# Kernel optimization log

Hardware: AMD Instinct MI355X
Metric: run time of the kernel (lower is better)

## Reference

```python
import jax, jax.numpy as jnp
import numpy as np

D = 1024
H = 16
MODES = 16
EPS = 1e-5


def _layernorm(x, g, b):
    mu = jnp.mean(x, axis=-1, keepdims=True)
    var = jnp.var(x, axis=-1, keepdims=True)
    return (x - mu) * jax.lax.rsqrt(var + EPS) * g + b


def setup_inputs() -> dict:
    key = jax.random.key(0)
    ks = jax.random.split(key, 12)
    B, S = 32, 2048
    x_feat = jax.random.normal(ks[0], (B, S, D), dtype=jnp.float32)
    z_prev = jax.random.normal(ks[1], (B, D), dtype=jnp.float32)
    # MultiheadAttention params (torch packs q,k,v in in_proj)
    in_proj_w = jax.random.normal(ks[2], (3 * D, D), dtype=jnp.float32) * (1.0 / np.sqrt(D))
    in_proj_b = jnp.zeros((3 * D,), dtype=jnp.float32)
    out_proj_w = jax.random.normal(ks[3], (D, D), dtype=jnp.float32) * (1.0 / np.sqrt(D))
    out_proj_b = jnp.zeros((D,), dtype=jnp.float32)
    ln1_g = jnp.ones((D,), jnp.float32); ln1_b = jnp.zeros((D,), jnp.float32)
    ln2_g = jnp.ones((D,), jnp.float32); ln2_b = jnp.zeros((D,), jnp.float32)
    scale_real = jax.random.normal(ks[4], (MODES, D), dtype=jnp.float32) * 0.02
    scale_imag = jax.random.normal(ks[5], (MODES, D), dtype=jnp.float32) * 0.02
    # spectral_norm(Linear): effective weight = W / sigma_max(W); bake it in
    Wp = np.asarray(jax.random.normal(ks[6], (D, D), dtype=jnp.float32)) * (1.0 / np.sqrt(D))
    sigma = np.linalg.svd(Wp, compute_uv=False)[0]
    proj_w = jnp.asarray(Wp / sigma, dtype=jnp.float32)
    proj_b = jnp.zeros((D,), jnp.float32)
    bn_g = jnp.ones((D,), jnp.float32); bn_b = jnp.zeros((D,), jnp.float32)
    gate = jnp.asarray(0.5, jnp.float32)
    scale_attn = jnp.ones((1,), jnp.float32)
    scale_denoise = jnp.ones((1,), jnp.float32)
    return dict(x_feat=x_feat, z_prev=z_prev, in_proj_w=in_proj_w, in_proj_b=in_proj_b,
                out_proj_w=out_proj_w, out_proj_b=out_proj_b, ln1_g=ln1_g, ln1_b=ln1_b,
                ln2_g=ln2_g, ln2_b=ln2_b, scale_real=scale_real, scale_imag=scale_imag,
                proj_w=proj_w, proj_b=proj_b, bn_g=bn_g, bn_b=bn_b, gate=gate,
                scale_attn=scale_attn, scale_denoise=scale_denoise)


def reference(x_feat, z_prev, in_proj_w, in_proj_b, out_proj_w, out_proj_b,
              ln1_g, ln1_b, ln2_g, ln2_b, scale_real, scale_imag,
              proj_w, proj_b, bn_g, bn_b, gate, scale_attn, scale_denoise):
    B, S, _ = x_feat.shape
    hd = D // H
    Wq, Wk, Wv = in_proj_w[:D], in_proj_w[D:2 * D], in_proj_w[2 * D:]
    bq, bk, bv = in_proj_b[:D], in_proj_b[D:2 * D], in_proj_b[2 * D:]
    # single-query cross attention: q from z_prev [B,D], k/v from x_feat [B,S,D]
    q = (z_prev @ Wq.T + bq).reshape(B, H, hd)
    k = (x_feat @ Wk.T + bk).reshape(B, S, H, hd)
    v = (x_feat @ Wv.T + bv).reshape(B, S, H, hd)
    scores = jnp.einsum('bhd,bshd->bhs', q, k) / np.sqrt(hd)
    attn = jax.nn.softmax(scores, axis=-1)
    ctx = jnp.einsum('bhs,bshd->bhd', attn, v).reshape(B, D)
    attn_out = ctx @ out_proj_w.T + out_proj_b
    z1 = _layernorm(z_prev + scale_attn * attn_out, ln1_g, ln1_b)  # [B,D]
    # fft_denoise: keep first MODES freqs, each scaled by mean of its complex filter row
    filt = jnp.mean(scale_real + 1j * scale_imag, axis=1)  # [MODES] complex
    fvec = jnp.zeros((D,), dtype=jnp.complex64).at[:MODES].set(filt.astype(jnp.complex64))
    z_freq = jnp.fft.fft(z1, axis=1) * fvec[None, :]
    z_spatial = jnp.fft.ifft(z_freq, axis=1).real.astype(z1.dtype)
    denoised = z_spatial @ proj_w.T + proj_b
    z2 = _layernorm(z1 + scale_denoise * denoised, ln2_g, ln2_b)
    g = jax.nn.sigmoid(gate)
    z3 = g * z2 + (1.0 - g) * z_prev
    # BatchNorm1d (training-mode batch stats, biased variance)
    mu = jnp.mean(z3, axis=0, keepdims=True)
    var = jnp.var(z3, axis=0, keepdims=True)
    out = (z3 - mu) * jax.lax.rsqrt(var + EPS) * bn_g + bn_b
    return out
```

## Files before the change

kernel.cpp:

```cpp
#include <hip/hip_runtime.h>
#include <hip/hip_bf16.h>

#define B_ 32
#define S_ 2048
#define D_ 1024
#define H_ 16
#define HD_ 64
#define MODES_ 16
#define EPS_ 1e-5f

#define NSPLIT_ 16
#define RPB_ 128
#define RPI_ 16
#define NIT_ (RPB_ / RPI_)

#define OFF_CK      32
#define OFF_Q       1024
#define OFF_QKBF    33792
#define OFF_ML      295936
#define ML_L_OFF    8192
#define OFF_PART_F  312320
#define OFF_CTX     4506624
#define OFF_R1      4539392
#define OFF_Z1      4572160
#define OFF_ZSP     4604928
#define OFF_R2      4637696
#define OFF_Z3      4670464

typedef __attribute__((ext_vector_type(8))) short short8v;
typedef __attribute__((ext_vector_type(4))) float f32x4;

static __device__ inline ushort2 f2bf2(float a, float b) {
    __hip_bfloat162 h = __float22bfloat162_rn(make_float2(a, b));
    union { __hip_bfloat162 h; ushort2 u; } v; v.h = h; return v.u;
}
static __device__ inline unsigned short f2bf(float a) {
    __hip_bfloat16 h = __float2bfloat16(a);
    union { __hip_bfloat16 h; unsigned short u; } v; v.h = h; return v.u;
}
static __device__ inline float bf2f(unsigned s) {
    union { unsigned u; float f; } v; v.u = s << 16;
    return v.f;
}

__global__ void k_q(const float* __restrict__ zprev, const float* __restrict__ ipw,
                    const float* __restrict__ ipb, float* __restrict__ q_out,
                    float* __restrict__ ck_out) {
    int b = blockIdx.x >> 2, nc = blockIdx.x & 3;
    __shared__ float zr[D_];
    int t = threadIdx.x;
    for (int i = t; i < D_; i += 256) zr[i] = zprev[(size_t)b * D_ + i];
    __syncthreads();
    int n = nc * 256 + t;
    const float4* wr = (const float4*)(ipw + (size_t)n * D_);
    float a0 = 0.f, a1 = 0.f, a2 = 0.f, a3 = 0.f;
    for (int k = 0; k < 256; k += 4) {
        float4 w0 = wr[k], w1 = wr[k + 1], w2 = wr[k + 2], w3 = wr[k + 3];
        float4 z0 = *(const float4*)&zr[4 * k];
        float4 z1 = *(const float4*)&zr[4 * k + 4];
        float4 z2 = *(const float4*)&zr[4 * k + 8];
        float4 z3 = *(const float4*)&zr[4 * k + 12];
        a0 = fmaf(z0.x, w0.x, a0); a0 = fmaf(z0.y, w0.y, a0); a0 = fmaf(z0.z, w0.z, a0); a0 = fmaf(z0.w, w0.w, a0);
        a1 = fmaf(z1.x, w1.x, a1); a1 = fmaf(z1.y, w1.y, a1); a1 = fmaf(z1.z, w1.z, a1); a1 = fmaf(z1.w, w1.w, a1);
        a2 = fmaf(z2.x, w2.x, a2); a2 = fmaf(z2.y, w2.y, a2); a2 = fmaf(z2.z, w2.z, a2); a2 = fmaf(z2.w, w2.w, a2);
        a3 = fmaf(z3.x, w3.x, a3); a3 = fmaf(z3.y, w3.y, a3); a3 = fmaf(z3.z, w3.z, a3); a3 = fmaf(z3.w, w3.w, a3);
    }
    float qv = (a0 + a1) + (a2 + a3) + ipb[n];
    q_out[(size_t)b * D_ + n] = qv;
    float cv = qv * ipb[D_ + n];
#pragma unroll
    for (int o = 32; o > 0; o >>= 1) cv += __shfl_xor(cv, o);
    if ((t & 63) == 0) ck_out[b * H_ + (n >> 6)] = cv;
}

__global__ void k_qkc(const float* __restrict__ ipw, const float* __restrict__ q_in,
                      unsigned short* __restrict__ qk_out) {
    int bid = blockIdx.x;
    int bc = bid & 3, nc = (bid >> 2) & 3, h = bid >> 4;
    int t = threadIdx.x;
    __shared__ float4 tile4[HD_ * 64];
    __shared__ float qall[8 * HD_];
    const float4* wk4 = (const float4*)(ipw + (size_t)D_ * D_);
#pragma unroll
    for (int j = 0; j < 16; ++j) {
        int lin4 = j * 256 + t;
        int i = lin4 >> 6, n4 = lin4 & 63;
        tile4[lin4] = wk4[(size_t)(h * HD_ + i) * 256 + nc * 64 + n4];
    }
#pragma unroll
    for (int j = 0; j < 2; ++j) {
        int idx = j * 256 + t;
        int bb = idx >> 6, i = idx & 63;
        qall[idx] = q_in[(size_t)(bc * 8 + bb) * D_ + h * HD_ + i];
    }
    __syncthreads();
    const float* tile = (const float*)tile4;
#pragma unroll
    for (int bb = 0; bb < 8; ++bb) {
        float a0 = 0.f, a1 = 0.f;
#pragma unroll
        for (int i = 0; i < HD_; i += 2) {
            a0 = fmaf(qall[bb * HD_ + i], tile[i * 256 + t], a0);
            a1 = fmaf(qall[bb * HD_ + i + 1], tile[(i + 1) * 256 + t], a1);
        }
        int b = bc * 8 + bb;
        qk_out[(size_t)(b * H_ + h) * D_ + nc * 256 + t] = f2bf(a0 + a1);
    }
}

__global__ __launch_bounds__(256, 2) void k_attn(const float* __restrict__ xfeat,
        const unsigned short* __restrict__ qkbf, const float* __restrict__ ck,
        unsigned short* __restrict__ part, float* __restrict__ ml) {
    int bid = blockIdx.x;
    int c = bid & (NSPLIT_ - 1), b = bid >> 4;
    int t = threadIdx.x, w = t >> 6, l = t & 63;
    __shared__ unsigned char xbuf[RPI_ * 2048];
    __shared__ unsigned char xcol[D_ * RPI_ * 2];
    __shared__ float Sred[4][RPI_][17];
    __shared__ unsigned short Pt[16][32];
    __shared__ float mh[16], lh[16], fh[16], ckl[16];

    if (t < 16) { mh[t] = -1e30f; lh[t] = 0.f; ckl[t] = ck[b * H_ + t]; }
    {
        int h = t >> 4, s = 16 + (t & 15);
        Pt[h][s] = 0;
    }

    f32x4 acc[16];
#pragma unroll
    for (int nt = 0; nt < 16; ++nt) acc[nt] = (f32x4){0.f, 0.f, 0.f, 0.f};

    int hr = l & 15, kg = l >> 4;
    const unsigned short* qkb = qkbf + ((size_t)(b * H_ + hr) << 10);
    short8v qfrag[8];
#pragma unroll
    for (int ks = 0; ks < 8; ++ks)
        qfrag[ks] = *(const short8v*)(qkb + w * 256 + ks * 32 + kg * 8);

    for (int it = 0; it < NIT_; ++it) {
        __syncthreads();
        {
            const float4* src = (const float4*)(xfeat + ((size_t)b * S_ + c * RPB_ + it * RPI_) * D_);
#pragma unroll
            for (int j = 0; j < 16; ++j) {
                int idx = j * 256 + t;
                float4 v = src[idx];
                int row = idx >> 8, dq = idx & 255;
                unsigned off = (unsigned)(row * 2048 + dq * 8) ^ (unsigned)((row & 7) << 4);
                ushort2 lo = f2bf2(v.x, v.y), hi = f2bf2(v.z, v.w);
                ushort4 u; u.x = lo.x; u.y = lo.y; u.z = hi.x; u.w = hi.y;
                *(ushort4*)(xbuf + off) = u;
            }
        }
        __syncthreads();
        {
            f32x4 s0 = {0.f, 0.f, 0.f, 0.f};
#pragma unroll
            for (int ks = 0; ks < 8; ++ks) {
                int k = w * 256 + ks * 32 + kg * 8;
                unsigned off0 = (unsigned)(hr * 2048 + k * 2) ^ (unsigned)((hr & 7) << 4);
                short8v a0 = *(const short8v*)(xbuf + off0);
                s0 = __builtin_amdgcn_mfma_f32_16x16x32_bf16(a0, qfrag[ks], s0, 0, 0, 0);
            }
            int rbase = kg * 4;
#pragma unroll
            for (int r = 0; r < 4; ++r) Sred[w][rbase + r][hr] = s0[r];
        }
        {
#pragma unroll
            for (int i = 0; i < 16; ++i) {
                int rg = i & 3, d = (i >> 2) * 256 + t;
                unsigned cb = (unsigned)((d >> 2) * 8) + (unsigned)((d & 3) * 2);
                int r0 = rg * 4;
                unsigned short v0 = *(const unsigned short*)(xbuf + (((unsigned)((r0 + 0) * 2048) + cb) ^ (unsigned)(((r0 + 0) & 7) << 4)));
                unsigned short v1 = *(const unsigned short*)(xbuf + (((unsigned)((r0 + 1) * 2048) + cb) ^ (unsigned)(((r0 + 1) & 7) << 4)));
                unsigned short v2 = *(const unsigned short*)(xbuf + (((unsigned)((r0 + 2) * 2048) + cb) ^ (unsigned)(((r0 + 2) & 7) << 4)));
                unsigned short v3 = *(const unsigned short*)(xbuf + (((unsigned)((r0 + 3) * 2048) + cb) ^ (unsigned)(((r0 + 3) & 7) << 4)));
                ushort4 u; u.x = v0; u.y = v1; u.z = v2; u.w = v3;
                unsigned slot = (unsigned)((rg >> 1) ^ ((d >> 2) & 1));
                unsigned coff = (unsigned)(d * 32) + slot * 16 + (unsigned)((rg & 1) * 8);
                *(ushort4*)(xcol + coff) = u;
            }
        }
        __syncthreads();
        {
            int h = t >> 4, i16 = t & 15;
            float sv0 = Sred[0][i16][h] + Sred[1][i16][h] + Sred[2][i16][h] + Sred[3][i16][h];
            float s0 = (sv0 + ckl[h]) * 0.125f;
            float mm = s0;
#pragma unroll
            for (int o = 8; o > 0; o >>= 1) mm = fmaxf(mm, __shfl_xor(mm, o, 16));
            float mold = mh[h];
            float mnew = fmaxf(mold, mm);
            float p0 = __expf(s0 - mnew);
            Pt[h][i16] = f2bf(p0);
            float ps = p0;
#pragma unroll
            for (int o = 8; o > 0; o >>= 1) ps += __shfl_xor(ps, o, 16);
            if (i16 == 0) {
                float f = __expf(mold - mnew);
                fh[h] = f; lh[h] = lh[h] * f + ps; mh[h] = mnew;
            }
        }
        __syncthreads();
        {
            float f0 = fh[kg * 4 + 0], f1 = fh[kg * 4 + 1], f2 = fh[kg * 4 + 2], f3 = fh[kg * 4 + 3];
#pragma unroll
            for (int nt = 0; nt < 16; ++nt) {
                acc[nt][0] *= f0; acc[nt][1] *= f1; acc[nt][2] *= f2; acc[nt][3] *= f3;
            }
            short8v pa = *(const short8v*)(&Pt[hr][kg * 8]);
#pragma unroll
            for (int nt = 0; nt < 16; ++nt) {
                int d = w * 256 + nt * 16 + hr;
                unsigned coff = (unsigned)(d * 32) + (unsigned)((((kg & 1) ^ ((d >> 2) & 1)) << 4));
                short8v bx = *(const short8v*)(xcol + coff);
                acc[nt] = __builtin_amdgcn_mfma_f32_16x16x32_bf16(pa, bx, acc[nt], 0, 0, 0);
            }
        }
    }
    {
#pragma unroll
        for (int nt = 0; nt < 16; ++nt) {
            int d = w * 256 + nt * 16 + hr;
#pragma unroll
            for (int r = 0; r < 4; ++r) {
                int h = kg * 4 + r;
                part[(((size_t)(c * B_ + b) * H_ + h) << 10) + d] = f2bf(acc[nt][r]);
            }
        }
        if (t < 16) {
            ml[(size_t)(c * B_ + b) * H_ + t] = mh[t];
            ml[ML_L_OFF + (size_t)(c * B_ + b) * H_ + t] = lh[t];
        }
    }
}

__global__ void k_ctx2(const float* __restrict__ ipw, const float* __restrict__ ipb,
                       const unsigned short* __restrict__ part, const float* __restrict__ ml,
                       float* __restrict__ ctx) {
    int b = blockIdx.x >> 2, nc = blockIdx.x & 3;
    int t = threadIdx.x;
    __shared__ float mls[4][16], lls[4][16], coef[4][16];
    __shared__ float xr[4 * D_];
    if (t < 64) {
        int h4 = t >> 4, c = t & 15;
        mls[h4][c] = ml[(size_t)(c * B_ + b) * H_ + nc * 4 + h4];
        lls[h4][c] = ml[ML_L_OFF + (size_t)(c * B_ + b) * H_ + nc * 4 + h4];
    }
    __syncthreads();
    if (t < 4) {
        float M = -1e30f;
        for (int c = 0; c < 16; ++c) M = fmaxf(M, mls[t][c]);
        float L = 0.f;
        for (int c = 0; c < 16; ++c) L += lls[t][c] * __expf(mls[t][c] - M);
        float invL = 1.f / L;
        for (int c = 0; c < 16; ++c) coef[t][c] = __expf(mls[t][c] - M) * invL;
    }
    __syncthreads();
    for (int idx = t * 2; idx < 4 * D_; idx += 512) {
        int h4 = idx >> 10, d = idx & 1023;
        int h = nc * 4 + h4;
        float a0 = 0.f, a1 = 0.f;
        for (int c = 0; c < 16; ++c) {
            unsigned u = *(const unsigned*)&part[(((size_t)(c * B_ + b) * H_ + h) << 10) + d];
            float cf = coef[h4][c];
            a0 = fmaf(bf2f(u & 0xffffu), cf, a0);
            a1 = fmaf(bf2f(u >> 16), cf, a1);
        }
        xr[idx] = a0; xr[idx + 1] = a1;
    }
    __syncthreads();
    int n = nc * 256 + t;
    int hl = t >> 6;
    const float4* wr = (const float4*)(ipw + ((size_t)2 * D_ + n) * D_);
    const float4* xv4 = (const float4*)&xr[hl * D_];
    float a0 = 0.f, a1 = 0.f, a2 = 0.f, a3 = 0.f;
    for (int k = 0; k < 256; k += 4) {
        float4 w0 = wr[k], w1 = wr[k + 1], w2 = wr[k + 2], w3 = wr[k + 3];
        float4 x0 = xv4[k], x1 = xv4[k + 1], x2 = xv4[k + 2], x3 = xv4[k + 3];
        a0 = fmaf(w0.x, x0.x, a0); a0 = fmaf(w0.y, x0.y, a0); a0 = fmaf(w0.z, x0.z, a0); a0 = fmaf(w0.w, x0.w, a0);
        a1 = fmaf(w1.x, x1.x, a1); a1 = fmaf(w1.y, x1.y, a1); a1 = fmaf(w1.z, x1.z, a1); a1 = fmaf(w1.w, x1.w, a1);
        a2 = fmaf(w2.x, x2.x, a2); a2 = fmaf(w2.y, x2.y, a2); a2 = fmaf(w2.z, x2.z, a2); a2 = fmaf(w2.w, x2.w, a2);
        a3 = fmaf(w3.x, x3.x, a3); a3 = fmaf(w3.y, x3.y, a3); a3 = fmaf(w3.z, x3.z, a3); a3 = fmaf(w3.w, x3.w, a3);
    }
    ctx[(size_t)b * D_ + n] = (a0 + a1) + (a2 + a3) + ipb[2 * D_ + n];
}

__global__ void k_proj_res(const float* __restrict__ wmat, const float* __restrict__ bias,
                           const float* __restrict__ scale, const float* __restrict__ resid,
                           const float* __restrict__ invec, float* __restrict__ outvec) {
    int b = blockIdx.x >> 2, nc = blockIdx.x & 3;
    __shared__ float cx[D_];
    int t = threadIdx.x;
    for (int i = t; i < D_; i += 256) cx[i] = invec[(size_t)b * D_ + i];
    __syncthreads();
    int n = nc * 256 + t;
    const float4* wr = (const float4*)(wmat + (size_t)n * D_);
    float a0 = 0.f, a1 = 0.f, a2 = 0.f, a3 = 0.f;
    for (int k = 0; k < 256; k += 4) {
        float4 w0 = wr[k], w1 = wr[k + 1], w2 = wr[k + 2], w3 = wr[k + 3];
        float4 c0 = *(const float4*)&cx[4 * k];
        float4 c1 = *(const float4*)&cx[4 * k + 4];
        float4 c2 = *(const float4*)&cx[4 * k + 8];
        float4 c3 = *(const float4*)&cx[4 * k + 12];
        a0 = fmaf(w0.x, c0.x, a0); a0 = fmaf(w0.y, c0.y, a0); a0 = fmaf(w0.z, c0.z, a0); a0 = fmaf(w0.w, c0.w, a0);
        a1 = fmaf(w1.x, c1.x, a1); a1 = fmaf(w1.y, c1.y, a1); a1 = fmaf(w1.z, c1.z, a1); a1 = fmaf(w1.w, c1.w, a1);
        a2 = fmaf(w2.x, c2.x, a2); a2 = fmaf(w2.y, c2.y, a2); a2 = fmaf(w2.z, c2.z, a2); a2 = fmaf(w2.w, c2.w, a2);
        a3 = fmaf(w3.x, c3.x, a3); a3 = fmaf(w3.y, c3.y, a3); a3 = fmaf(w3.z, c3.z, a3); a3 = fmaf(w3.w, c3.w, a3);
    }
    float acc = (a0 + a1) + (a2 + a3);
    outvec[(size_t)b * D_ + n] = resid[(size_t)b * D_ + n] + scale[0] * (acc + bias[n]);
}

__global__ void k_lnspec(const float* __restrict__ r1, const float* __restrict__ g1,
                         const float* __restrict__ b1, const float* __restrict__ sreal,
                         const float* __restrict__ simag, float* __restrict__ z1out,
                         float* __restrict__ zspout) {
    int b = blockIdx.x, t = threadIdx.x, w = t >> 6, l = t & 63;
    __shared__ float zr[D_];
    __shared__ float fre[MODES_], fim[MODES_];
    __shared__ float cre[MODES_], cim[MODES_];
    __shared__ float sa[4], sb[4];
    float4 v = ((const float4*)(r1 + (size_t)b * D_))[t];
    float s = v.x + v.y + v.z + v.w;
    float s2 = v.x * v.x + v.y * v.y + v.z * v.z + v.w * v.w;
#pragma unroll
    for (int o = 32; o > 0; o >>= 1) { s += __shfl_xor(s, o); s2 += __shfl_xor(s2, o); }
    if (l == 0) { sa[w] = s; sb[w] = s2; }
    int m = t >> 4, sub = t & 15;
    {
        float ar = 0.f, ai = 0.f;
        for (int k = sub; k < D_; k += 16) { ar += sreal[m * D_ + k]; ai += simag[m * D_ + k]; }
#pragma unroll
        for (int o = 8; o > 0; o >>= 1) { ar += __shfl_xor(ar, o, 16); ai += __shfl_xor(ai, o, 16); }
        if (sub == 0) { fre[m] = ar * (1.f / (float)D_); fim[m] = ai * (1.f / (float)D_); }
    }
    __syncthreads();
    s = sa[0] + sa[1] + sa[2] + sa[3];
    s2 = sb[0] + sb[1] + sb[2] + sb[3];
    float mu = s * (1.f / (float)D_);
    float var = s2 * (1.f / (float)D_) - mu * mu;
    float rs = rsqrtf(var + EPS_);
    float4 gg = ((const float4*)g1)[t], bbv = ((const float4*)b1)[t];
    float4 z4;
    z4.x = (v.x - mu) * rs * gg.x + bbv.x;
    z4.y = (v.y - mu) * rs * gg.y + bbv.y;
    z4.z = (v.z - mu) * rs * gg.z + bbv.z;
    z4.w = (v.w - mu) * rs * gg.w + bbv.w;
    ((float4*)(z1out + (size_t)b * D_))[t] = z4;
    *(float4*)&zr[4 * t] = z4;
    __syncthreads();
    const float step = 6.283185307179586f / (float)D_;
    {
        float ar = 0.f, ai = 0.f;
        for (int n = sub; n < D_; n += 16) {
            int idx = (m * n) & (D_ - 1);
            float sn, cs;
            __sincosf(step * (float)idx, &sn, &cs);
            float z = zr[n];
            ar = fmaf(z, cs, ar); ai = fmaf(-z, sn, ai);
        }
#pragma unroll
        for (int o = 8; o > 0; o >>= 1) { ar += __shfl_xor(ar, o, 16); ai += __shfl_xor(ai, o, 16); }
        if (sub == 0) {
            cre[m] = (fre[m] * ar - fim[m] * ai) * (1.f / (float)D_);
            cim[m] = (fre[m] * ai + fim[m] * ar) * (1.f / (float)D_);
        }
    }
    __syncthreads();
    for (int n = t; n < D_; n += 256) {
        float acc = 0.f;
#pragma unroll
        for (int mm = 0; mm < MODES_; ++mm) {
            int idx = (mm * n) & (D_ - 1);
            float sn, cs;
            __sincosf(step * (float)idx, &sn, &cs);
            acc += cre[mm] * cs - cim[mm] * sn;
        }
        zspout[(size_t)b * D_ + n] = acc;
    }
}

__global__ void k_ln2gate(const float* __restrict__ zprev, const float* __restrict__ g2,
                          const float* __restrict__ b2v, const float* __restrict__ gate,
                          float* __restrict__ ws) {
    int b = blockIdx.x, t = threadIdx.x, w = t >> 6, l = t & 63;
    float4 v = ((const float4*)(ws + OFF_R2 + (size_t)b * D_))[t];
    float s = v.x + v.y + v.z + v.w;
    float s2 = v.x * v.x + v.y * v.y + v.z * v.z + v.w * v.w;
    __shared__ float sa[4], sb[4];
#pragma unroll
    for (int o = 32; o > 0; o >>= 1) { s += __shfl_xor(s, o); s2 += __shfl_xor(s2, o); }
    if (l == 0) { sa[w] = s; sb[w] = s2; }
    __syncthreads();
    s = sa[0] + sa[1] + sa[2] + sa[3];
    s2 = sb[0] + sb[1] + sb[2] + sb[3];
    float mu = s * (1.f / (float)D_);
    float var = s2 * (1.f / (float)D_) - mu * mu;
    float rs = rsqrtf(var + EPS_);
    float4 gg = ((const float4*)g2)[t], bb = ((const float4*)b2v)[t];
    float gsig = 1.f / (1.f + __expf(-gate[0]));
    float4 zp = ((const float4*)(zprev + (size_t)b * D_))[t];
    float4 z3;
    z3.x = gsig * ((v.x - mu) * rs * gg.x + bb.x) + (1.f - gsig) * zp.x;
    z3.y = gsig * ((v.y - mu) * rs * gg.y + bb.y) + (1.f - gsig) * zp.y;
    z3.z = gsig * ((v.z - mu) * rs * gg.z + bb.z) + (1.f - gsig) * zp.z;
    z3.w = gsig * ((v.w - mu) * rs * gg.w + bb.w) + (1.f - gsig) * zp.w;
    ((float4*)(ws + OFF_Z3 + (size_t)b * D_))[t] = z3;
}

__global__ void k_bn(const float* __restrict__ bng, const float* __restrict__ bnb,
                     const float* __restrict__ z3, float* __restrict__ out) {
    int d = blockIdx.x * 256 + threadIdx.x;
    float vals[B_];
    float s = 0.f, s2 = 0.f;
#pragma unroll
    for (int b = 0; b < B_; ++b) {
        float v = z3[(size_t)b * D_ + d];
        vals[b] = v; s += v; s2 = fmaf(v, v, s2);
    }
    float mu = s * (1.f / (float)B_);
    float var = s2 * (1.f / (float)B_) - mu * mu;
    float rs = rsqrtf(var + EPS_);
    float gg = bng[d], bb = bnb[d];
#pragma unroll
    for (int b = 0; b < B_; ++b) out[(size_t)b * D_ + d] = (vals[b] - mu) * rs * gg + bb;
}

extern "C" void kernel_launch(void* const* d_in, const int* in_sizes, int n_in,
                              void* d_out, int out_size, void* d_ws, size_t ws_size,
                              hipStream_t stream) {
    const float* x_feat = (const float*)d_in[0];
    const float* z_prev = (const float*)d_in[1];
    const float* ipw    = (const float*)d_in[2];
    const float* ipb    = (const float*)d_in[3];
    const float* wout   = (const float*)d_in[4];
    const float* bout   = (const float*)d_in[5];
    const float* ln1g   = (const float*)d_in[6];
    const float* ln1b   = (const float*)d_in[7];
    const float* ln2g   = (const float*)d_in[8];
    const float* ln2b   = (const float*)d_in[9];
    const float* sreal  = (const float*)d_in[10];
    const float* simag  = (const float*)d_in[11];
    const float* pw     = (const float*)d_in[12];
    const float* pb     = (const float*)d_in[13];
    const float* bng    = (const float*)d_in[14];
    const float* bnb    = (const float*)d_in[15];
    const float* gate   = (const float*)d_in[16];
    const float* sattn  = (const float*)d_in[17];
    const float* sden   = (const float*)d_in[18];
    float* ws  = (float*)d_ws;
    float* out = (float*)d_out;
    unsigned short* qkbf  = (unsigned short*)(ws + OFF_QKBF);
    unsigned short* partp = (unsigned short*)(ws + OFF_PART_F);

    k_q<<<B_ * 4, 256, 0, stream>>>(z_prev, ipw, ipb, ws + OFF_Q, ws + OFF_CK);
    k_qkc<<<H_ * 16, 256, 0, stream>>>(ipw, ws + OFF_Q, qkbf);
    k_attn<<<B_ * NSPLIT_, 256, 0, stream>>>(x_feat, qkbf, ws + OFF_CK, partp, ws + OFF_ML);
    k_ctx2<<<B_ * 4, 256, 0, stream>>>(ipw, ipb, partp, ws + OFF_ML, ws + OFF_CTX);
    k_proj_res<<<B_ * 4, 256, 0, stream>>>(wout, bout, sattn, z_prev, ws + OFF_CTX, ws + OFF_R1);
    k_lnspec<<<B_, 256, 0, stream>>>(ws + OFF_R1, ln1g, ln1b, sreal, simag,
                                     ws + OFF_Z1, ws + OFF_ZSP);
    k_proj_res<<<B_ * 4, 256, 0, stream>>>(pw, pb, sden, ws + OFF_Z1, ws + OFF_ZSP, ws + OFF_R2);
    k_ln2gate<<<B_, 256, 0, stream>>>(z_prev, ln2g, ln2b, gate, ws);
    k_bn<<<D_ / 256, 256, 0, stream>>>(bng, bnb, ws + OFF_Z3, out);
}
```

Measured before the change: 224.1 us.

## Widen attention and GEMV kernels to 512 threads, prefetch next x tile into registers

The split-K attention kernel now runs 8 waves per block, each covering half the previous K/D slice. It loads the next 16-row x_feat tile into registers while the current tile is converted and consumed, so global loads overlap compute. The ctx and projection GEMV kernels also move to 512 threads, splitting each dot product across two lanes joined with a shuffle. The aim is more memory parallelism and latency hiding, at the cost of extra register pressure from the prefetch buffer, an 8-way Sred reduction, and a launch bound of 4 blocks per SM that may be hard to meet with shared memory use.

```diff
diff --git a/kernel.cpp b/kernel.cpp
--- a/kernel.cpp
+++ b/kernel.cpp
@@ -108,7 +108,7 @@
     }
 }
 
-__global__ __launch_bounds__(256, 2) void k_attn(const float* __restrict__ xfeat,
+__global__ __launch_bounds__(512, 4) void k_attn(const float* __restrict__ xfeat,
         const unsigned short* __restrict__ qkbf, const float* __restrict__ ck,
         unsigned short* __restrict__ part, float* __restrict__ ml) {
     int bid = blockIdx.x;
@@ -116,48 +116,54 @@
     int t = threadIdx.x, w = t >> 6, l = t & 63;
     __shared__ unsigned char xbuf[RPI_ * 2048];
     __shared__ unsigned char xcol[D_ * RPI_ * 2];
-    __shared__ float Sred[4][RPI_][17];
+    __shared__ float Sred[8][RPI_][17];
     __shared__ unsigned short Pt[16][32];
     __shared__ float mh[16], lh[16], fh[16], ckl[16];
 
     if (t < 16) { mh[t] = -1e30f; lh[t] = 0.f; ckl[t] = ck[b * H_ + t]; }
-    {
+    if (t < 256) {
         int h = t >> 4, s = 16 + (t & 15);
         Pt[h][s] = 0;
     }
 
-    f32x4 acc[16];
-#pragma unroll
-    for (int nt = 0; nt < 16; ++nt) acc[nt] = (f32x4){0.f, 0.f, 0.f, 0.f};
+    f32x4 acc[8];
+#pragma unroll
+    for (int nt = 0; nt < 8; ++nt) acc[nt] = (f32x4){0.f, 0.f, 0.f, 0.f};
 
     int hr = l & 15, kg = l >> 4;
     const unsigned short* qkb = qkbf + ((size_t)(b * H_ + hr) << 10);
-    short8v qfrag[8];
-#pragma unroll
-    for (int ks = 0; ks < 8; ++ks)
-        qfrag[ks] = *(const short8v*)(qkb + w * 256 + ks * 32 + kg * 8);
+    short8v qfrag[4];
+#pragma unroll
+    for (int ks = 0; ks < 4; ++ks)
+        qfrag[ks] = *(const short8v*)(qkb + w * 128 + ks * 32 + kg * 8);
+
+    const float4* xbase = (const float4*)(xfeat + ((size_t)b * S_ + c * RPB_) * D_);
+    float4 cur[8];
+#pragma unroll
+    for (int j = 0; j < 8; ++j) cur[j] = xbase[j * 512 + t];
 
     for (int it = 0; it < NIT_; ++it) {
         __syncthreads();
-        {
-            const float4* src = (const float4*)(xfeat + ((size_t)b * S_ + c * RPB_ + it * RPI_) * D_);
-#pragma unroll
-            for (int j = 0; j < 16; ++j) {
-                int idx = j * 256 + t;
-                float4 v = src[idx];
-                int row = idx >> 8, dq = idx & 255;
-                unsigned off = (unsigned)(row * 2048 + dq * 8) ^ (unsigned)((row & 7) << 4);
-                ushort2 lo = f2bf2(v.x, v.y), hi = f2bf2(v.z, v.w);
-                ushort4 u; u.x = lo.x; u.y = lo.y; u.z = hi.x; u.w = hi.y;
-                *(ushort4*)(xbuf + off) = u;
-            }
+#pragma unroll
+        for (int j = 0; j < 8; ++j) {
+            int idx = j * 512 + t;
+            int row = idx >> 8, dq = idx & 255;
+            unsigned off = (unsigned)(row * 2048 + dq * 8) ^ (unsigned)((row & 7) << 4);
+            ushort2 lo = f2bf2(cur[j].x, cur[j].y), hi = f2bf2(cur[j].z, cur[j].w);
+            ushort4 u; u.x = lo.x; u.y = lo.y; u.z = hi.x; u.w = hi.y;
+            *(ushort4*)(xbuf + off) = u;
+        }
+        if (it + 1 < NIT_) {
+            const float4* src = xbase + (size_t)(it + 1) * (RPI_ * D_ / 4);
+#pragma unroll
+            for (int j = 0; j < 8; ++j) cur[j] = src[j * 512 + t];
         }
         __syncthreads();
         {
             f32x4 s0 = {0.f, 0.f, 0.f, 0.f};
 #pragma unroll
-            for (int ks = 0; ks < 8; ++ks) {
-                int k = w * 256 + ks * 32 + kg * 8;
+            for (int ks = 0; ks < 4; ++ks) {
+                int k = w * 128 + ks * 32 + kg * 8;
                 unsigned off0 = (unsigned)(hr * 2048 + k * 2) ^ (unsigned)((hr & 7) << 4);
                 short8v a0 = *(const short8v*)(xbuf + off0);
                 s0 = __builtin_amdgcn_mfma_f32_16x16x32_bf16(a0, qfrag[ks], s0, 0, 0, 0);
@@ -168,8 +174,8 @@
         }
         {
 #pragma unroll
-            for (int i = 0; i < 16; ++i) {
-                int rg = i & 3, d = (i >> 2) * 256 + t;
+            for (int i = 0; i < 8; ++i) {
+                int rg = i >> 1, d = (i & 1) * 512 + t;
                 unsigned cb = (unsigned)((d >> 2) * 8) + (unsigned)((d & 3) * 2);
                 int r0 = rg * 4;
                 unsigned short v0 = *(const unsigned short*)(xbuf + (((unsigned)((r0 + 0) * 2048) + cb) ^ (unsigned)(((r0 + 0) & 7) << 4)));
@@ -183,9 +189,11 @@
             }
         }
         __syncthreads();
-        {
+        if (t < 256) {
             int h = t >> 4, i16 = t & 15;
-            float sv0 = Sred[0][i16][h] + Sred[1][i16][h] + Sred[2][i16][h] + Sred[3][i16][h];
+            float sv0 = 0.f;
+#pragma unroll
+            for (int ww = 0; ww < 8; ++ww) sv0 += Sred[ww][i16][h];
             float s0 = (sv0 + ckl[h]) * 0.125f;
             float mm = s0;
 #pragma unroll
@@ -206,13 +214,13 @@
         {
             float f0 = fh[kg * 4 + 0], f1 = fh[kg * 4 + 1], f2 = fh[kg * 4 + 2], f3 = fh[kg * 4 + 3];
 #pragma unroll
-            for (int nt = 0; nt < 16; ++nt) {
+            for (int nt = 0; nt < 8; ++nt) {
                 acc[nt][0] *= f0; acc[nt][1] *= f1; acc[nt][2] *= f2; acc[nt][3] *= f3;
             }
             short8v pa = *(const short8v*)(&Pt[hr][kg * 8]);
 #pragma unroll
-            for (int nt = 0; nt < 16; ++nt) {
-                int d = w * 256 + nt * 16 + hr;
+            for (int nt = 0; nt < 8; ++nt) {
+                int d = w * 128 + nt * 16 + hr;
                 unsigned coff = (unsigned)(d * 32) + (unsigned)((((kg & 1) ^ ((d >> 2) & 1)) << 4));
                 short8v bx = *(const short8v*)(xcol + coff);
                 acc[nt] = __builtin_amdgcn_mfma_f32_16x16x32_bf16(pa, bx, acc[nt], 0, 0, 0);
@@ -221,8 +229,8 @@
     }
     {
 #pragma unroll
-        for (int nt = 0; nt < 16; ++nt) {
-            int d = w * 256 + nt * 16 + hr;
+        for (int nt = 0; nt < 8; ++nt) {
+            int d = w * 128 + nt * 16 + hr;
 #pragma unroll
             for (int r = 0; r < 4; ++r) {
                 int h = kg * 4 + r;
@@ -258,7 +266,7 @@
         for (int c = 0; c < 16; ++c) coef[t][c] = __expf(mls[t][c] - M) * invL;
     }
     __syncthreads();
-    for (int idx = t * 2; idx < 4 * D_; idx += 512) {
+    for (int idx = t * 2; idx < 4 * D_; idx += 1024) {
         int h4 = idx >> 10, d = idx & 1023;
         int h = nc * 4 + h4;
         float a0 = 0.f, a1 = 0.f;
@@ -271,12 +279,12 @@
         xr[idx] = a0; xr[idx + 1] = a1;
     }
     __syncthreads();
-    int n = nc * 256 + t;
-    int hl = t >> 6;
-    const float4* wr = (const float4*)(ipw + ((size_t)2 * D_ + n) * D_);
-    const float4* xv4 = (const float4*)&xr[hl * D_];
+    int n = nc * 256 + (t >> 1), half = t & 1;
+    int hl = t >> 7;
+    const float4* wr = (const float4*)(ipw + ((size_t)2 * D_ + n) * D_) + half * 128;
+    const float4* xv4 = (const float4*)&xr[hl * D_] + half * 128;
     float a0 = 0.f, a1 = 0.f, a2 = 0.f, a3 = 0.f;
-    for (int k = 0; k < 256; k += 4) {
+    for (int k = 0; k < 128; k += 4) {
         float4 w0 = wr[k], w1 = wr[k + 1], w2 = wr[k + 2], w3 = wr[k + 3];
         float4 x0 = xv4[k], x1 = xv4[k + 1], x2 = xv4[k + 2], x3 = xv4[k + 3];
         a0 = fmaf(w0.x, x0.x, a0); a0 = fmaf(w0.y, x0.y, a0); a0 = fmaf(w0.z, x0.z, a0); a0 = fmaf(w0.w, x0.w, a0);
@@ -284,7 +292,9 @@
         a2 = fmaf(w2.x, x2.x, a2); a2 = fmaf(w2.y, x2.y, a2); a2 = fmaf(w2.z, x2.z, a2); a2 = fmaf(w2.w, x2.w, a2);
         a3 = fmaf(w3.x, x3.x, a3); a3 = fmaf(w3.y, x3.y, a3); a3 = fmaf(w3.z, x3.z, a3); a3 = fmaf(w3.w, x3.w, a3);
     }
-    ctx[(size_t)b * D_ + n] = (a0 + a1) + (a2 + a3) + ipb[2 * D_ + n];
+    float acc = (a0 + a1) + (a2 + a3);
+    acc += __shfl_xor(acc, 1);
+    if (half == 0) ctx[(size_t)b * D_ + n] = acc + ipb[2 * D_ + n];
 }
 
 __global__ void k_proj_res(const float* __restrict__ wmat, const float* __restrict__ bias,
@@ -293,24 +303,24 @@
     int b = blockIdx.x >> 2, nc = blockIdx.x & 3;
     __shared__ float cx[D_];
     int t = threadIdx.x;
-    for (int i = t; i < D_; i += 256) cx[i] = invec[(size_t)b * D_ + i];
-    __syncthreads();
-    int n = nc * 256 + t;
-    const float4* wr = (const float4*)(wmat + (size_t)n * D_);
+    for (int i = t; i < D_; i += 512) cx[i] = invec[(size_t)b * D_ + i];
+    __syncthreads();
+    int n = nc * 256 + (t >> 1), half = t & 1;
+    const float4* wr = (const float4*)(wmat + (size_t)n * D_) + half * 128;
+    const float4* cv4 = (const float4*)cx + half * 128;
     float a0 = 0.f, a1 = 0.f, a2 = 0.f, a3 = 0.f;
-    for (int k = 0; k < 256; k += 4) {
+    for (int k = 0; k < 128; k += 4) {
         float4 w0 = wr[k], w1 = wr[k + 1], w2 = wr[k + 2], w3 = wr[k + 3];
-        float4 c0 = *(const float4*)&cx[4 * k];
-        float4 c1 = *(const float4*)&cx[4 * k + 4];
-        float4 c2 = *(const float4*)&cx[4 * k + 8];
-        float4 c3 = *(const float4*)&cx[4 * k + 12];
+        float4 c0 = cv4[k], c1 = cv4[k + 1], c2 = cv4[k + 2], c3 = cv4[k + 3];
         a0 = fmaf(w0.x, c0.x, a0); a0 = fmaf(w0.y, c0.y, a0); a0 = fmaf(w0.z, c0.z, a0); a0 = fmaf(w0.w, c0.w, a0);
         a1 = fmaf(w1.x, c1.x, a1); a1 = fmaf(w1.y, c1.y, a1); a1 = fmaf(w1.z, c1.z, a1); a1 = fmaf(w1.w, c1.w, a1);
         a2 = fmaf(w2.x, c2.x, a2); a2 = fmaf(w2.y, c2.y, a2); a2 = fmaf(w2.z, c2.z, a2); a2 = fmaf(w2.w, c2.w, a2);
         a3 = fmaf(w3.x, c3.x, a3); a3 = fmaf(w3.y, c3.y, a3); a3 = fmaf(w3.z, c3.z, a3); a3 = fmaf(w3.w, c3.w, a3);
     }
     float acc = (a0 + a1) + (a2 + a3);
-    outvec[(size_t)b * D_ + n] = resid[(size_t)b * D_ + n] + scale[0] * (acc + bias[n]);
+    acc += __shfl_xor(acc, 1);
+    if (half == 0)
+        outvec[(size_t)b * D_ + n] = resid[(size_t)b * D_ + n] + scale[0] * (acc + bias[n]);
 }
 
 __global__ void k_lnspec(const float* __restrict__ r1, const float* __restrict__ g1,
@@ -457,12 +467,12 @@
 
     k_q<<<B_ * 4, 256, 0, stream>>>(z_prev, ipw, ipb, ws + OFF_Q, ws + OFF_CK);
     k_qkc<<<H_ * 16, 256, 0, stream>>>(ipw, ws + OFF_Q, qkbf);
-    k_attn<<<B_ * NSPLIT_, 256, 0, stream>>>(x_feat, qkbf, ws + OFF_CK, partp, ws + OFF_ML);
-    k_ctx2<<<B_ * 4, 256, 0, stream>>>(ipw, ipb, partp, ws + OFF_ML, ws + OFF_CTX);
-    k_proj_res<<<B_ * 4, 256, 0, stream>>>(wout, bout, sattn, z_prev, ws + OFF_CTX, ws + OFF_R1);
+    k_attn<<<B_ * NSPLIT_, 512, 0, stream>>>(x_feat, qkbf, ws + OFF_CK, partp, ws + OFF_ML);
+    k_ctx2<<<B_ * 4, 512, 0, stream>>>(ipw, ipb, partp, ws + OFF_ML, ws + OFF_CTX);
+    k_proj_res<<<B_ * 4, 512, 0, stream>>>(wout, bout, sattn, z_prev, ws + OFF_CTX, ws + OFF_R1);
     k_lnspec<<<B_, 256, 0, stream>>>(ws + OFF_R1, ln1g, ln1b, sreal, simag,
                                      ws + OFF_Z1, ws + OFF_ZSP);
-    k_proj_res<<<B_ * 4, 256, 0, stream>>>(pw, pb, sden, ws + OFF_Z1, ws + OFF_ZSP, ws + OFF_R2);
+    k_proj_res<<<B_ * 4, 512, 0, stream>>>(pw, pb, sden, ws + OFF_Z1, ws + OFF_ZSP, ws + OFF_R2);
     k_ln2gate<<<B_, 256, 0, stream>>>(z_prev, ln2g, ln2b, gate, ws);
     k_bn<<<D_ / 256, 256, 0, stream>>>(bng, bnb, ws + OFF_Z3, out);
 }
```

New measurement: 254.1 us. +13.4%, slower.
